# Kernel optimization log

Hardware: AMD Instinct MI355X
Metric: run time of the kernel (lower is better)

The kernel has to match this reference:

```python
import jax, jax.numpy as jnp
import numpy as np

N_NODES = 100000
N_EDGES = 3200000
N_IN = 128
N_OUT = 64
ITERATIONS = 150
LEAK = 0.01


def _mml_activation(v):
    # piecewise: leaky below 0, Michaelis-Menten-like saturation above 0.5
    v = jnp.where(v < 0, v * LEAK, v)
    safe = jnp.where(v > 0.5, v, 1.0)  # avoid div-by-zero on untaken branch
    return jnp.where(v > 0.5, 1.0 - 0.25 / safe, v)


def setup_inputs() -> dict:
    key = jax.random.key(0)
    ks = jax.random.split(key, 9)
    x = jax.random.normal(ks[0], (1, N_IN), dtype=jnp.float32)
    in_weights = jnp.ones((N_IN,), jnp.float32)  # inputAmplitude * ones
    # weights init: 0.1 + 0.1*U, sign flipped for inhibitory reactions
    mag = 0.1 + 0.1 * jax.random.uniform(ks[1], (N_EDGES,), dtype=jnp.float32)
    sign = jnp.where(jax.random.bernoulli(ks[2], 0.5, (N_EDGES,)), 1.0, -1.0)
    rec_weights = mag * sign
    biases = 0.001 * jnp.ones((N_NODES,), jnp.float32)
    out_weights = jnp.ones((N_OUT,), jnp.float32)  # projectionAmplitude * ones
    in_indices = jax.random.randint(ks[3], (N_IN,), 0, N_NODES, dtype=jnp.int32)
    edge_rows = jax.random.randint(ks[4], (N_EDGES,), 0, N_NODES, dtype=jnp.int32)
    edge_cols = jax.random.randint(ks[5], (N_EDGES,), 0, N_NODES, dtype=jnp.int32)
    out_indices = jax.random.randint(ks[6], (N_OUT,), 0, N_NODES, dtype=jnp.int32)
    return {"x": x, "in_weights": in_weights, "rec_weights": rec_weights,
            "biases": biases, "out_weights": out_weights,
            "in_indices": in_indices, "edge_rows": edge_rows,
            "edge_cols": edge_cols, "out_indices": out_indices}


def reference(x, in_weights, rec_weights, biases, out_weights,
              in_indices, edge_rows, edge_cols, out_indices):
    # input projection: scatter weighted inputs into node vector [N_NODES]
    node_in = jnp.zeros((N_NODES,), x.dtype).at[in_indices].set(in_weights * x[0])
    b_in = node_in + biases

    def step(y, _):
        # sparse matvec A @ y: gather sources, weight, scatter-add to rows
        s = jax.ops.segment_sum(rec_weights * y[edge_cols], edge_rows,
                                num_segments=N_NODES)
        return _mml_activation(s + b_in), None

    y0 = jnp.zeros((N_NODES,), x.dtype)
    y, _ = jax.lax.scan(step, y0, None, length=ITERATIONS)
    # output projection: gather + scale -> [1, N_OUT]
    return (out_weights * y[out_indices])[None, :]
```

## Files before the change

kernel.cpp:

```cpp
#include <hip/hip_runtime.h>

#define N_NODES 100000
#define N_EDGES 3200000
#define N_IN    128
#define N_OUT   64
#define ITERS   150
#define LEAK    0.01f

#define NB      256
#define NT      1024
#define RPB     391
#define NQ      4
#define QSZ     25000
#define NKEYS   (N_NODES * NQ)
#define SCAN_CHUNK 1024
#define SCAN_NBLK  391
#define NEPOCH  64
#define EPOCH_STRIDE 32
#define YSTR    100096

__device__ __forceinline__ float mml(float v) {
    v = (v < 0.0f) ? v * LEAK : v;
    if (v > 0.5f) v = 1.0f - 0.25f / v;
    return v;
}

__global__ void k_binit(const float* __restrict__ biases, float* __restrict__ b_in) {
    int i = blockIdx.x * blockDim.x + threadIdx.x;
    if (i < N_NODES) b_in[i] = biases[i];
}

__global__ void k_scatter_in(const float* __restrict__ x,
                             const float* __restrict__ in_w,
                             const int*   __restrict__ in_idx,
                             const float* __restrict__ biases,
                             float* __restrict__ b_in) {
    int k = threadIdx.x;
    if (k < N_IN) {
        int idx = in_idx[k];
        bool last = true;
        for (int j = k + 1; j < N_IN; ++j)
            if (in_idx[j] == idx) { last = false; break; }
        if (last) b_in[idx] = biases[idx] + in_w[k] * x[k];
    }
}

__global__ void k_y0(const float* __restrict__ b_in, float* __restrict__ y0) {
    int i = blockIdx.x * blockDim.x + threadIdx.x;
    if (i < N_NODES) y0[i] = mml(b_in[i]);
}

__global__ void k_hist(const int* __restrict__ rows, const int* __restrict__ cols,
                       int* __restrict__ counts) {
    int i = blockIdx.x * blockDim.x + threadIdx.x;
    int stride = gridDim.x * blockDim.x;
    for (; i < N_EDGES; i += stride) {
        int key = rows[i] * NQ + cols[i] / QSZ;
        atomicAdd(&counts[key], 1);
    }
}

__global__ void k_scan1(const int* __restrict__ counts, int* __restrict__ rp,
                        int* __restrict__ blockSums) {
    __shared__ int sm[SCAN_CHUNK];
    int t = threadIdx.x;
    int i = blockIdx.x * SCAN_CHUNK + t;
    int v = (i < NKEYS) ? counts[i] : 0;
    sm[t] = v;
    __syncthreads();
    for (int off = 1; off < SCAN_CHUNK; off <<= 1) {
        int add = (t >= off) ? sm[t - off] : 0;
        __syncthreads();
        sm[t] += add;
        __syncthreads();
    }
    if (i <= NKEYS) rp[i] = sm[t] - v;
    if (t == SCAN_CHUNK - 1) blockSums[blockIdx.x] = sm[t];
}

__global__ void k_scan2(int* __restrict__ blockSums) {
    __shared__ int sm[512];
    int t = threadIdx.x;
    int v = (t < SCAN_NBLK) ? blockSums[t] : 0;
    sm[t] = v;
    __syncthreads();
    for (int off = 1; off < 512; off <<= 1) {
        int add = (t >= off) ? sm[t - off] : 0;
        __syncthreads();
        sm[t] += add;
        __syncthreads();
    }
    if (t < SCAN_NBLK) blockSums[t] = sm[t] - v;
}

__global__ void k_scan3(int* __restrict__ rp, const int* __restrict__ blockSums,
                        int* __restrict__ next) {
    int i = blockIdx.x * SCAN_CHUNK + threadIdx.x;
    if (i <= NKEYS) {
        int val = rp[i] + blockSums[blockIdx.x];
        rp[i] = val;
        if (i < NKEYS) next[i] = val;
    }
}

__global__ void k_scatter_edges(const int* __restrict__ rows, const int* __restrict__ cols,
                                const float* __restrict__ w,
                                int* __restrict__ next, int2* __restrict__ csr) {
    int i = blockIdx.x * blockDim.x + threadIdx.x;
    int stride = gridDim.x * blockDim.x;
    for (; i < N_EDGES; i += stride) {
        int c = cols[i];
        int q = c / QSZ;
        int key = rows[i] * NQ + q;
        int p = atomicAdd(&next[key], 1);
        csr[p] = make_int2(c - q * QSZ, __float_as_int(w[i]));
    }
}

__device__ __forceinline__ float segsum(const int* __restrict__ rp2,
                                        const int2* __restrict__ csr,
                                        const float* __restrict__ sy,
                                        int row, int q, int j) {
    const int key = row * NQ + q;
    int e = rp2[key] + j;
    const int end = rp2[key + 1];
    float a0 = 0.f, a1 = 0.f;
    for (; e + 4 < end; e += 8) {
        int2 c0 = csr[e];
        int2 c1 = csr[e + 4];
        a0 += __int_as_float(c0.y) * sy[c0.x];
        a1 += __int_as_float(c1.y) * sy[c1.x];
    }
    if (e < end) {
        int2 c = csr[e];
        a0 += __int_as_float(c.y) * sy[c.x];
    }
    return a0 + a1;
}

__global__ __launch_bounds__(NT) void k_iterate(
    const int*  __restrict__ rp2,
    const int2* __restrict__ csr,
    const float* __restrict__ b_in,
    float* __restrict__ ybufs,
    int* __restrict__ arr,
    int* __restrict__ epoch,
    const int* __restrict__ out_idx,
    const float* __restrict__ out_w,
    float* __restrict__ out,
    int nbuf, int sc1mode)
{
    __shared__ float sy[QSZ];
    const int b = blockIdx.x, t = threadIdx.x;
    const int nb = gridDim.x;
    const int g = t >> 2, j = t & 3;
    const int row0 = b * RPB;
    const int row_end = (row0 + RPB < N_NODES) ? row0 + RPB : N_NODES;
    const int r1 = row0 + g;
    const int r2 = row0 + g + 256;

    for (int it = 1; it < ITERS; ++it) {
        const float* ysrc = ybufs + (size_t)((it - 1) % nbuf) * YSTR;
        float*       ydst = ybufs + (size_t)(it % nbuf) * YSTR;
        float acc1 = 0.f, acc2 = 0.f;
        #pragma unroll
        for (int q = 0; q < NQ; ++q) {
            if (!sc1mode) {
                const float4* src = (const float4*)(ysrc + q * QSZ);
                #pragma unroll
                for (int i = 0; i < 7; ++i) {
                    int idx = t + i * NT;
                    if (idx < QSZ / 4) ((float4*)sy)[idx] = src[idx];
                }
            } else {
                const float* src = ysrc + q * QSZ;
                #pragma unroll
                for (int i = 0; i < 25; ++i) {
                    int idx = t + i * NT;
                    if (idx < QSZ)
                        sy[idx] = __hip_atomic_load(&src[idx], __ATOMIC_RELAXED,
                                                    __HIP_MEMORY_SCOPE_AGENT);
                }
            }
            __syncthreads();
            if (r1 < row_end) acc1 += segsum(rp2, csr, sy, r1, q, j);
            if (r2 < row_end) acc2 += segsum(rp2, csr, sy, r2, q, j);
            __syncthreads();
        }
        acc1 += __shfl_xor(acc1, 1); acc1 += __shfl_xor(acc1, 2);
        acc2 += __shfl_xor(acc2, 1); acc2 += __shfl_xor(acc2, 2);
        if (j == 0) {
            if (r1 < row_end)
                __hip_atomic_store(&ydst[r1], mml(b_in[r1] + acc1),
                                   __ATOMIC_RELAXED, __HIP_MEMORY_SCOPE_AGENT);
            if (r2 < row_end)
                __hip_atomic_store(&ydst[r2], mml(b_in[r2] + acc2),
                                   __ATOMIC_RELAXED, __HIP_MEMORY_SCOPE_AGENT);
        }
        __syncthreads();

        if (t == 0)
            __hip_atomic_store(&arr[b], it, __ATOMIC_RELEASE,
                               __HIP_MEMORY_SCOPE_AGENT);
        if (b == 0) {
            if (t < 64) {
                int ok;
                do {
                    ok = 1;
                    #pragma unroll
                    for (int k = 0; k < 4; ++k) {
                        int bb = t + k * 64;
                        if (bb < nb)
                            ok &= (__hip_atomic_load(&arr[bb], __ATOMIC_RELAXED,
                                     __HIP_MEMORY_SCOPE_AGENT) >= it);
                    }
                    if (!ok) __builtin_amdgcn_s_sleep(1);
                } while (!__all(ok));
                __hip_atomic_store(&epoch[t * EPOCH_STRIDE], it,
                                   __ATOMIC_RELAXED, __HIP_MEMORY_SCOPE_AGENT);
            }
            __syncthreads();
        } else {
            if (t == 0) {
                while (__hip_atomic_load(&epoch[(b & (NEPOCH - 1)) * EPOCH_STRIDE],
                         __ATOMIC_RELAXED, __HIP_MEMORY_SCOPE_AGENT) < it)
                    __builtin_amdgcn_s_sleep(2);
            }
            __syncthreads();
        }
        asm volatile("" ::: "memory");
    }

    if (b == 0 && t < N_OUT) {
        const float* yfin = ybufs + (size_t)((ITERS - 1) % nbuf) * YSTR;
        out[t] = out_w[t] * __hip_atomic_load(&yfin[out_idx[t]],
                   __ATOMIC_RELAXED, __HIP_MEMORY_SCOPE_AGENT);
    }
}

extern "C" void kernel_launch(void* const* d_in, const int* in_sizes, int n_in,
                              void* d_out, int out_size, void* d_ws, size_t ws_size,
                              hipStream_t stream) {
    const float* x      = (const float*)d_in[0];
    const float* in_w   = (const float*)d_in[1];
    const float* rec_w  = (const float*)d_in[2];
    const float* biases = (const float*)d_in[3];
    const float* out_w  = (const float*)d_in[4];
    const int*   in_idx = (const int*)d_in[5];
    const int*   e_rows = (const int*)d_in[6];
    const int*   e_cols = (const int*)d_in[7];
    const int*   out_idx= (const int*)d_in[8];
    float* out = (float*)d_out;

    char* ws = (char*)d_ws;
    float* b_in    = (float*)ws;
    int*   rp2     = (int*)(b_in + N_NODES);
    int*   counts  = rp2 + (NKEYS + 64);
    int*   blockSums = counts + NKEYS;
    int*   arr     = blockSums + 512;
    int*   epoch   = arr + NB;
    size_t off = (size_t)((char*)(epoch + NEPOCH * EPOCH_STRIDE) - ws);
    off = (off + 255) & ~(size_t)255;
    int2* csr = (int2*)(ws + off);
    size_t off2 = off + (size_t)N_EDGES * sizeof(int2);
    off2 = (off2 + 255) & ~(size_t)255;
    float* ybufs = (float*)(ws + off2);

    size_t fullA = off2 + (size_t)150 * YSTR * sizeof(float);
    int nbuf, sc1mode;
    if (ws_size >= fullA) { nbuf = 150; sc1mode = 0; }
    else                  { nbuf = 2;   sc1mode = 1; }

    hipMemsetAsync(counts, 0, NKEYS * sizeof(int), stream);
    hipMemsetAsync(arr, 0, (NB + NEPOCH * EPOCH_STRIDE) * sizeof(int), stream);

    k_binit<<<391, 256, 0, stream>>>(biases, b_in);
    k_scatter_in<<<1, 128, 0, stream>>>(x, in_w, in_idx, biases, b_in);
    k_y0<<<391, 256, 0, stream>>>(b_in, ybufs);

    k_hist<<<1024, 256, 0, stream>>>(e_rows, e_cols, counts);
    k_scan1<<<SCAN_NBLK, SCAN_CHUNK, 0, stream>>>(counts, rp2, blockSums);
    k_scan2<<<1, 512, 0, stream>>>(blockSums);
    k_scan3<<<SCAN_NBLK, SCAN_CHUNK, 0, stream>>>(rp2, blockSums, counts);
    k_scatter_edges<<<1024, 256, 0, stream>>>(e_rows, e_cols, rec_w, counts, csr);

    int*   rp_a   = rp2;
    int2*  csr_a  = csr;
    float* bin_a  = b_in;
    float* yb_a   = ybufs;
    int*   arr_a  = arr;
    int*   ep_a   = epoch;
    const int*   oidx_a = out_idx;
    const float* ow_a   = out_w;
    float* out_a  = out;
    void* args[] = { &rp_a, &csr_a, &bin_a, &yb_a, &arr_a, &ep_a,
                     &oidx_a, &ow_a, &out_a, &nbuf, &sc1mode };
    hipLaunchCooperativeKernel((void*)k_iterate, dim3(NB), dim3(NT),
                               args, 0, stream);
}
```

Baseline: 3.112 ms.

## Replace grid barrier with per-chunk dataflow gating and double-buffered LDS chunks

The single grid-wide barrier per iteration is replaced by a dedicated coordinator block that publishes per-column-chunk readiness epochs. Worker blocks start on a column chunk of the previous iteration's vector as soon as the blocks producing that chunk have finished. The column space is split into 8 chunks, double-buffered in shared memory, with the next chunk prefetched while the current one is processed. CSR keys are reordered chunk-major, which doubles the size of the scan. The aim is to cut barrier stalls and overlap loads with compute, at the cost of more gating overhead and one block spent only on coordination.

```diff
diff --git a/kernel.cpp b/kernel.cpp
--- a/kernel.cpp
+++ b/kernel.cpp
@@ -7,17 +7,21 @@
 #define ITERS   150
 #define LEAK    0.01f
 
-#define NB      256
+#define NBW     254
+#define NBLK    (NBW + 1)
 #define NT      1024
-#define RPB     391
-#define NQ      4
-#define QSZ     25000
-#define NKEYS   (N_NODES * NQ)
+#define RPB     394
+#define NCH     8
+#define CH      12544
+#define CHF4    (CH / 4)
+#define LASTF4  3048
+#define NKEYS   (NCH * N_NODES)
 #define SCAN_CHUNK 1024
-#define SCAN_NBLK  391
-#define NEPOCH  64
-#define EPOCH_STRIDE 32
+#define SCAN_NBLK  782
+#define NEPC    16
+#define EPST    32
 #define YSTR    100096
+#define NBUF    150
 
 __device__ __forceinline__ float mml(float v) {
     v = (v < 0.0f) ? v * LEAK : v;
@@ -55,7 +59,7 @@
     int i = blockIdx.x * blockDim.x + threadIdx.x;
     int stride = gridDim.x * blockDim.x;
     for (; i < N_EDGES; i += stride) {
-        int key = rows[i] * NQ + cols[i] / QSZ;
+        int key = (cols[i] / CH) * N_NODES + rows[i];
         atomicAdd(&counts[key], 1);
     }
 }
@@ -79,12 +83,12 @@
 }
 
 __global__ void k_scan2(int* __restrict__ blockSums) {
-    __shared__ int sm[512];
+    __shared__ int sm[1024];
     int t = threadIdx.x;
     int v = (t < SCAN_NBLK) ? blockSums[t] : 0;
     sm[t] = v;
     __syncthreads();
-    for (int off = 1; off < 512; off <<= 1) {
+    for (int off = 1; off < 1024; off <<= 1) {
         int add = (t >= off) ? sm[t - off] : 0;
         __syncthreads();
         sm[t] += add;
@@ -110,32 +114,24 @@
     int stride = gridDim.x * blockDim.x;
     for (; i < N_EDGES; i += stride) {
         int c = cols[i];
-        int q = c / QSZ;
-        int key = rows[i] * NQ + q;
+        int g = c / CH;
+        int key = g * N_NODES + rows[i];
         int p = atomicAdd(&next[key], 1);
-        csr[p] = make_int2(c - q * QSZ, __float_as_int(w[i]));
-    }
-}
-
-__device__ __forceinline__ float segsum(const int* __restrict__ rp2,
-                                        const int2* __restrict__ csr,
-                                        const float* __restrict__ sy,
-                                        int row, int q, int j) {
-    const int key = row * NQ + q;
-    int e = rp2[key] + j;
-    const int end = rp2[key + 1];
-    float a0 = 0.f, a1 = 0.f;
-    for (; e + 4 < end; e += 8) {
-        int2 c0 = csr[e];
-        int2 c1 = csr[e + 4];
-        a0 += __int_as_float(c0.y) * sy[c0.x];
-        a1 += __int_as_float(c1.y) * sy[c1.x];
-    }
-    if (e < end) {
-        int2 c = csr[e];
-        a0 += __int_as_float(c.y) * sy[c.x];
-    }
-    return a0 + a1;
+        csr[p] = make_int2(c - g * CH, __float_as_int(w[i]));
+    }
+}
+
+__device__ __forceinline__ void gate(int g, int it, int b, int t,
+                                     const int* __restrict__ epoch,
+                                     volatile int* s_rdy) {
+    if (t == 0) {
+        const int c = b & (NEPC - 1);
+        while (__hip_atomic_load(&epoch[(g * NEPC + c) * EPST], __ATOMIC_RELAXED,
+                                 __HIP_MEMORY_SCOPE_AGENT) < it - 1)
+            __builtin_amdgcn_s_sleep(1);
+        s_rdy[g] = it;
+    }
+    while (s_rdy[g] < it) {}
 }
 
 __global__ __launch_bounds__(NT) void k_iterate(
@@ -150,91 +146,143 @@
     float* __restrict__ out,
     int nbuf, int sc1mode)
 {
-    __shared__ float sy[QSZ];
+    __shared__ float syA[CH], syB[CH];
+    __shared__ int s_rdy_s[NCH];
+    volatile int* s_rdy = s_rdy_s;
     const int b = blockIdx.x, t = threadIdx.x;
-    const int nb = gridDim.x;
-    const int g = t >> 2, j = t & 3;
-    const int row0 = b * RPB;
+
+    if (b == 0) {
+        if (t < NCH * 64) {
+            const int g = t >> 6, k = t & 63;
+            const int c0 = g * CH;
+            const int c1 = ((c0 + CH < N_NODES) ? c0 + CH : N_NODES) - 1;
+            const int wf = c0 / RPB, wl = c1 / RPB;
+            const int sz = wl - wf + 1;
+            for (int v = 1; v <= ITERS - 1; ++v) {
+                if (k < sz) {
+                    while (__hip_atomic_load(&arr[wf + 1 + k], __ATOMIC_RELAXED,
+                                             __HIP_MEMORY_SCOPE_AGENT) < v)
+                        __builtin_amdgcn_s_sleep(2);
+                }
+                if (k < NEPC)
+                    __hip_atomic_store(&epoch[(g * NEPC + k) * EPST], v,
+                                       __ATOMIC_RELAXED, __HIP_MEMORY_SCOPE_AGENT);
+            }
+        }
+        return;
+    }
+
+    const int wi = b - 1;
+    const int row0 = wi * RPB;
     const int row_end = (row0 + RPB < N_NODES) ? row0 + RPB : N_NODES;
-    const int r1 = row0 + g;
-    const int r2 = row0 + g + 256;
-
-    for (int it = 1; it < ITERS; ++it) {
+    const int gq = t >> 2, j = t & 3;
+    const int r1 = row0 + gq;
+    const int r2 = row0 + gq + 256;
+
+    if (t < NCH) s_rdy_s[t] = 0;
+    __syncthreads();
+
+    for (int it = 1; it <= ITERS - 1; ++it) {
         const float* ysrc = ybufs + (size_t)((it - 1) % nbuf) * YSTR;
         float*       ydst = ybufs + (size_t)(it % nbuf) * YSTR;
         float acc1 = 0.f, acc2 = 0.f;
-        #pragma unroll
-        for (int q = 0; q < NQ; ++q) {
-            if (!sc1mode) {
-                const float4* src = (const float4*)(ysrc + q * QSZ);
-                #pragma unroll
-                for (int i = 0; i < 7; ++i) {
-                    int idx = t + i * NT;
-                    if (idx < QSZ / 4) ((float4*)sy)[idx] = src[idx];
-                }
-            } else {
-                const float* src = ysrc + q * QSZ;
-                #pragma unroll
-                for (int i = 0; i < 25; ++i) {
-                    int idx = t + i * NT;
-                    if (idx < QSZ)
-                        sy[idx] = __hip_atomic_load(&src[idx], __ATOMIC_RELAXED,
+
+        gate(0, it, b, t, epoch, s_rdy);
+        if (!sc1mode) {
+            float4 R[4];
+            const float4* s4 = (const float4*)ysrc;
+            #pragma unroll
+            for (int r = 0; r < 4; ++r) { int idx = t + r * NT; if (idx < CHF4) R[r] = s4[idx]; }
+            float4* d4 = (float4*)syA;
+            #pragma unroll
+            for (int r = 0; r < 4; ++r) { int idx = t + r * NT; if (idx < CHF4) d4[idx] = R[r]; }
+        } else {
+            for (int idx = t; idx < CH; idx += NT)
+                syA[idx] = __hip_atomic_load(&ysrc[idx], __ATOMIC_RELAXED,
+                                             __HIP_MEMORY_SCOPE_AGENT);
+        }
+        __syncthreads();
+
+        for (int g = 0; g < NCH; ++g) {
+            const float* sy = (g & 1) ? syB : syA;
+            const int gn = g + 1;
+            float4 R[4];
+            int n4n = 0;
+            if (gn < NCH) {
+                gate(gn, it, b, t, epoch, s_rdy);
+                n4n = (gn == NCH - 1) ? LASTF4 : CHF4;
+                if (!sc1mode) {
+                    const float4* s4 = (const float4*)(ysrc + (size_t)gn * CH);
+                    #pragma unroll
+                    for (int r = 0; r < 4; ++r) { int idx = t + r * NT; if (idx < n4n) R[r] = s4[idx]; }
+                }
+            }
+            {
+                const int key = g * N_NODES + r1;
+                int e = rp2[key] + j;
+                const int end = rp2[key + 1];
+                for (; e < end; e += 4) {
+                    int2 cc = csr[e];
+                    acc1 += __int_as_float(cc.y) * sy[cc.x];
+                }
+            }
+            if (r2 < row_end) {
+                const int key = g * N_NODES + r2;
+                int e = rp2[key] + j;
+                const int end = rp2[key + 1];
+                for (; e < end; e += 4) {
+                    int2 cc = csr[e];
+                    acc2 += __int_as_float(cc.y) * sy[cc.x];
+                }
+            }
+            if (gn < NCH) {
+                float4* d4 = (float4*)((gn & 1) ? syB : syA);
+                if (!sc1mode) {
+                    #pragma unroll
+                    for (int r = 0; r < 4; ++r) { int idx = t + r * NT; if (idx < n4n) d4[idx] = R[r]; }
+                } else {
+                    const float* src = ysrc + (size_t)gn * CH;
+                    int chn = n4n * 4;
+                    for (int idx = t; idx < chn; idx += NT)
+                        d4[0] = d4[0];
+                    float* df = (float*)d4;
+                    for (int idx = t; idx < chn; idx += NT)
+                        df[idx] = __hip_atomic_load(&src[idx], __ATOMIC_RELAXED,
                                                     __HIP_MEMORY_SCOPE_AGENT);
                 }
             }
             __syncthreads();
-            if (r1 < row_end) acc1 += segsum(rp2, csr, sy, r1, q, j);
-            if (r2 < row_end) acc2 += segsum(rp2, csr, sy, r2, q, j);
-            __syncthreads();
-        }
+        }
+
         acc1 += __shfl_xor(acc1, 1); acc1 += __shfl_xor(acc1, 2);
         acc2 += __shfl_xor(acc2, 1); acc2 += __shfl_xor(acc2, 2);
         if (j == 0) {
-            if (r1 < row_end)
-                __hip_atomic_store(&ydst[r1], mml(b_in[r1] + acc1),
-                                   __ATOMIC_RELAXED, __HIP_MEMORY_SCOPE_AGENT);
+            __hip_atomic_store(&ydst[r1], mml(b_in[r1] + acc1),
+                               __ATOMIC_RELAXED, __HIP_MEMORY_SCOPE_AGENT);
             if (r2 < row_end)
                 __hip_atomic_store(&ydst[r2], mml(b_in[r2] + acc2),
                                    __ATOMIC_RELAXED, __HIP_MEMORY_SCOPE_AGENT);
         }
         __syncthreads();
-
         if (t == 0)
             __hip_atomic_store(&arr[b], it, __ATOMIC_RELEASE,
                                __HIP_MEMORY_SCOPE_AGENT);
-        if (b == 0) {
-            if (t < 64) {
-                int ok;
-                do {
-                    ok = 1;
-                    #pragma unroll
-                    for (int k = 0; k < 4; ++k) {
-                        int bb = t + k * 64;
-                        if (bb < nb)
-                            ok &= (__hip_atomic_load(&arr[bb], __ATOMIC_RELAXED,
-                                     __HIP_MEMORY_SCOPE_AGENT) >= it);
-                    }
-                    if (!ok) __builtin_amdgcn_s_sleep(1);
-                } while (!__all(ok));
-                __hip_atomic_store(&epoch[t * EPOCH_STRIDE], it,
-                                   __ATOMIC_RELAXED, __HIP_MEMORY_SCOPE_AGENT);
-            }
-            __syncthreads();
-        } else {
-            if (t == 0) {
-                while (__hip_atomic_load(&epoch[(b & (NEPOCH - 1)) * EPOCH_STRIDE],
-                         __ATOMIC_RELAXED, __HIP_MEMORY_SCOPE_AGENT) < it)
-                    __builtin_amdgcn_s_sleep(2);
-            }
-            __syncthreads();
-        }
-        asm volatile("" ::: "memory");
-    }
-
-    if (b == 0 && t < N_OUT) {
-        const float* yfin = ybufs + (size_t)((ITERS - 1) % nbuf) * YSTR;
-        out[t] = out_w[t] * __hip_atomic_load(&yfin[out_idx[t]],
-                   __ATOMIC_RELAXED, __HIP_MEMORY_SCOPE_AGENT);
+    }
+
+    if (b == 1) {
+        if (t == 0) {
+            const int c = b & (NEPC - 1);
+            for (int g = 0; g < NCH; ++g)
+                while (__hip_atomic_load(&epoch[(g * NEPC + c) * EPST], __ATOMIC_RELAXED,
+                                         __HIP_MEMORY_SCOPE_AGENT) < ITERS - 1)
+                    __builtin_amdgcn_s_sleep(1);
+        }
+        __syncthreads();
+        if (t < N_OUT) {
+            const float* yfin = ybufs + (size_t)((ITERS - 1) % nbuf) * YSTR;
+            out[t] = out_w[t] * __hip_atomic_load(&yfin[out_idx[t]], __ATOMIC_RELAXED,
+                                                  __HIP_MEMORY_SCOPE_AGENT);
+        }
     }
 }
 
@@ -257,22 +305,22 @@
     int*   rp2     = (int*)(b_in + N_NODES);
     int*   counts  = rp2 + (NKEYS + 64);
     int*   blockSums = counts + NKEYS;
-    int*   arr     = blockSums + 512;
-    int*   epoch   = arr + NB;
-    size_t off = (size_t)((char*)(epoch + NEPOCH * EPOCH_STRIDE) - ws);
+    int*   arr     = blockSums + 1024;
+    int*   epoch   = arr + 256;
+    size_t off = (size_t)((char*)(epoch + NCH * NEPC * EPST) - ws);
     off = (off + 255) & ~(size_t)255;
     int2* csr = (int2*)(ws + off);
     size_t off2 = off + (size_t)N_EDGES * sizeof(int2);
     off2 = (off2 + 255) & ~(size_t)255;
     float* ybufs = (float*)(ws + off2);
 
-    size_t fullA = off2 + (size_t)150 * YSTR * sizeof(float);
+    size_t fullA = off2 + (size_t)NBUF * YSTR * sizeof(float);
     int nbuf, sc1mode;
-    if (ws_size >= fullA) { nbuf = 150; sc1mode = 0; }
-    else                  { nbuf = 2;   sc1mode = 1; }
+    if (ws_size >= fullA) { nbuf = NBUF; sc1mode = 0; }
+    else                  { nbuf = 2;    sc1mode = 1; }
 
     hipMemsetAsync(counts, 0, NKEYS * sizeof(int), stream);
-    hipMemsetAsync(arr, 0, (NB + NEPOCH * EPOCH_STRIDE) * sizeof(int), stream);
+    hipMemsetAsync(arr, 0, (256 + NCH * NEPC * EPST) * sizeof(int), stream);
 
     k_binit<<<391, 256, 0, stream>>>(biases, b_in);
     k_scatter_in<<<1, 128, 0, stream>>>(x, in_w, in_idx, biases, b_in);
@@ -280,7 +328,7 @@
 
     k_hist<<<1024, 256, 0, stream>>>(e_rows, e_cols, counts);
     k_scan1<<<SCAN_NBLK, SCAN_CHUNK, 0, stream>>>(counts, rp2, blockSums);
-    k_scan2<<<1, 512, 0, stream>>>(blockSums);
+    k_scan2<<<1, 1024, 0, stream>>>(blockSums);
     k_scan3<<<SCAN_NBLK, SCAN_CHUNK, 0, stream>>>(rp2, blockSums, counts);
     k_scatter_edges<<<1024, 256, 0, stream>>>(e_rows, e_cols, rec_w, counts, csr);
 
@@ -295,6 +343,6 @@
     float* out_a  = out;
     void* args[] = { &rp_a, &csr_a, &bin_a, &yb_a, &arr_a, &ep_a,
                      &oidx_a, &ow_a, &out_a, &nbuf, &sc1mode };
-    hipLaunchCooperativeKernel((void*)k_iterate, dim3(NB), dim3(NT),
+    hipLaunchCooperativeKernel((void*)k_iterate, dim3(NBLK), dim3(NT),
                                args, 0, stream);
 }
```

Result: slower. 6.430 ms (+106.6%).
